# Kernel optimization log

Hardware: AMD Instinct MI355X
Metric: run time of the kernel (lower is better)

## Reference

```python
import jax, jax.numpy as jnp
import numpy as np

N, E, F, FE, H, R = 100000, 3200000, 2, 7, 64, 500
BN_EPS = 1e-5
LEAKY_SLOPE = 0.01


def _bn(h, g, b):
    # BatchNorm1d in training mode: batch statistics over the node axis
    m = h.mean(0)
    v = h.var(0)
    return (h - m) * jax.lax.rsqrt(v + BN_EPS) * g + b


def _gine_conv(x, src, dst, edge_attr, eps, el_w, el_b, w1, b1, g, bt, w2, b2):
    # message: relu(x_j + Lin(edge_attr)); aggregate: scatter-add at dst
    msg = jax.nn.relu(x[src] + edge_attr @ el_w + el_b)          # [E, d]
    agg = jax.ops.segment_sum(msg, dst, num_segments=N)          # [N, d]
    h = (1.0 + eps) * x + agg
    # nn: Linear -> BN -> ReLU -> Linear -> ReLU
    h = jax.nn.relu(_bn(h @ w1 + b1, g, bt))
    return jax.nn.relu(h @ w2 + b2)


def setup_inputs() -> dict:
    key = jax.random.key(0)
    ks = jax.random.split(key, 16)
    r = lambda k, s, sc=0.1: jax.random.normal(k, s, dtype=jnp.float32) * sc
    return {
        "x": jax.random.normal(ks[0], (N, F), dtype=jnp.float32),
        "edge_attr": jax.random.normal(ks[1], (E, FE), dtype=jnp.float32),
        "edge_index": jax.random.randint(ks[2], (2, E), 0, N),
        "epoch": 1,
        "eps1": jnp.zeros((), jnp.float32),
        "el1_w": r(ks[3], (FE, F)), "el1_b": jnp.zeros((F,), jnp.float32),
        "n1_w1": r(ks[4], (F, H)), "n1_b1": jnp.zeros((H,), jnp.float32),
        "n1_g": jnp.ones((H,), jnp.float32), "n1_bt": jnp.zeros((H,), jnp.float32),
        "n1_w2": r(ks[5], (H, H)), "n1_b2": jnp.zeros((H,), jnp.float32),
        "eps2": jnp.zeros((), jnp.float32),
        "el2_w": r(ks[6], (FE, H)), "el2_b": jnp.zeros((H,), jnp.float32),
        "n2_w1": r(ks[7], (H, H)), "n2_b1": jnp.zeros((H,), jnp.float32),
        "n2_g": jnp.ones((H,), jnp.float32), "n2_bt": jnp.zeros((H,), jnp.float32),
        "n2_w2": r(ks[8], (H, H)), "n2_b2": jnp.zeros((H,), jnp.float32),
        "reg_w": r(ks[9], (H, R)), "reg_b": jnp.zeros((R,), jnp.float32),
        "end_w": r(ks[10], (R, 1)), "end_b": jnp.zeros((1,), jnp.float32),
    }


def reference(x, edge_attr, edge_index, epoch,
              eps1, el1_w, el1_b, n1_w1, n1_b1, n1_g, n1_bt, n1_w2, n1_b2,
              eps2, el2_w, el2_b, n2_w1, n2_b1, n2_g, n2_bt, n2_w2, n2_b2,
              reg_w, reg_b, end_w, end_b):
    src, dst = edge_index[0], edge_index[1]
    out = _gine_conv(x, src, dst, edge_attr, eps1, el1_w, el1_b,
                     n1_w1, n1_b1, n1_g, n1_bt, n1_w2, n1_b2)
    for _ in range(3 - 1):  # num_layers=3, shared conv2 weights
        out = _gine_conv(out, src, dst, edge_attr, eps2, el2_w, el2_b,
                         n2_w1, n2_b1, n2_g, n2_bt, n2_w2, n2_b2)
    # dropout p=0.0 -> identity; epoch only resets dropout, no effect here
    out = out @ reg_w + reg_b
    out = jnp.where(out >= 0, out, LEAKY_SLOPE * out)  # LeakyReLU
    out = out @ end_w + end_b                            # [N, 1]
    return out
```

## Files before the change

kernel.cpp:

```cpp
#include <hip/hip_runtime.h>

#define NN 100000
#define NE 3200000

__global__ __launch_bounds__(256) void count_kernel(const int* __restrict__ dst,
                                                    int* __restrict__ cnt) {
  int stride = gridDim.x * 256;
  for (int e = blockIdx.x * 256 + threadIdx.x; e < NE; e += stride)
    atomicAdd(&cnt[dst[e]], 1);
}

__global__ __launch_bounds__(1024) void scan_kernel(const int* __restrict__ cnt,
                                                    int* __restrict__ rowptr,
                                                    int* __restrict__ ofs) {
  __shared__ int bsum[1024];
  int tid = threadIdx.x;
  const int CH = (NN + 1023) / 1024;
  int lo = tid * CH, hi = lo + CH < NN ? lo + CH : NN;
  if (lo > NN) lo = NN;
  if (hi < lo) hi = lo;
  int s = 0;
  for (int i = lo; i < hi; i++) s += cnt[i];
  bsum[tid] = s;
  __syncthreads();
  for (int off = 1; off < 1024; off <<= 1) {
    int v = bsum[tid];
    int u = (tid >= off) ? bsum[tid - off] : 0;
    __syncthreads();
    bsum[tid] = v + u;
    __syncthreads();
  }
  int pre = (tid == 0) ? 0 : bsum[tid - 1];
  for (int i = lo; i < hi; i++) {
    int cv = cnt[i];
    rowptr[i] = pre;
    ofs[i] = pre;
    pre += cv;
  }
  if (tid == 1023) rowptr[NN] = pre;
}

__global__ __launch_bounds__(256) void scatter2p_kernel(
    const int* __restrict__ src, const int* __restrict__ dst,
    const float* __restrict__ ea, int* __restrict__ ofs,
    float* __restrict__ pe, const float* __restrict__ x,
    const float* __restrict__ elw, const float* __restrict__ elb,
    float* __restrict__ msg1) {
  float w0[7], w1r[7];
#pragma unroll
  for (int k = 0; k < 7; k++) { w0[k] = elw[k * 2]; w1r[k] = elw[k * 2 + 1]; }
  float b0 = elb[0], b1 = elb[1];
  int stride = gridDim.x * 256;
  for (int e = blockIdx.x * 256 + threadIdx.x; e < NE; e += stride) {
    int sn = src[e];
    int pos = atomicAdd(&ofs[dst[e]], 1);
    float av[7];
#pragma unroll
    for (int k = 0; k < 7; k++) av[k] = ea[e * 7 + k];
    float4 a, b;
    a.x = av[0]; a.y = av[1]; a.z = av[2]; a.w = av[3];
    b.x = av[4]; b.y = av[5]; b.z = av[6];
    b.w = __int_as_float(sn);
    ((float4*)pe)[pos * 2 + 0] = a;
    ((float4*)pe)[pos * 2 + 1] = b;
    float m0 = b0, m1 = b1;
#pragma unroll
    for (int k = 0; k < 7; k++) {
      m0 = fmaf(av[k], w0[k], m0);
      m1 = fmaf(av[k], w1r[k], m1);
    }
    m0 = fmaxf(m0 + x[sn * 2 + 0], 0.f);
    m1 = fmaxf(m1 + x[sn * 2 + 1], 0.f);
    float2 mv; mv.x = m0; mv.y = m1;
    ((float2*)msg1)[pos] = mv;
  }
}

__global__ __launch_bounds__(256) void scatter1_kernel(
    const int* __restrict__ dst, int* __restrict__ ofs, int* __restrict__ eid_s) {
  int stride = gridDim.x * 256;
  for (int e = blockIdx.x * 256 + threadIdx.x; e < NE; e += stride) {
    int pos = atomicAdd(&ofs[dst[e]], 1);
    eid_s[pos] = e;
  }
}

__global__ __launch_bounds__(256) void l1sum_kernel(
    const int* __restrict__ rowptr, const float* __restrict__ msg1,
    float* __restrict__ agg) {
  int stride = gridDim.x * 256;
  for (int n = blockIdx.x * 256 + threadIdx.x; n < NN; n += stride) {
    int r0 = rowptr[n], r1 = rowptr[n + 1];
    float a0 = 0.f, a1 = 0.f;
    const float2* mp = (const float2*)msg1;
    for (int i = r0; i < r1; i++) {
      float2 v = mp[i];
      a0 += v.x;
      a1 += v.y;
    }
    agg[n * 2 + 0] = a0;
    agg[n * 2 + 1] = a1;
  }
}

__global__ __launch_bounds__(256) void l1agg_kernel(
    const int* __restrict__ rowptr, const int* __restrict__ eid_s,
    const int* __restrict__ src, const float* __restrict__ ea,
    const float* __restrict__ x, const float* __restrict__ elw,
    const float* __restrict__ elb, float* __restrict__ agg) {
  float w0[7], w1r[7];
#pragma unroll
  for (int k = 0; k < 7; k++) { w0[k] = elw[k * 2]; w1r[k] = elw[k * 2 + 1]; }
  float b0 = elb[0], b1 = elb[1];
  int stride = gridDim.x * 256;
  for (int n = blockIdx.x * 256 + threadIdx.x; n < NN; n += stride) {
    int r0 = rowptr[n], r1 = rowptr[n + 1];
    float a0 = 0.f, a1 = 0.f;
    for (int i = r0; i < r1; i++) {
      int e = eid_s[i];
      int sn = src[e];
      float m0 = b0, m1 = b1;
#pragma unroll
      for (int k = 0; k < 7; k++) {
        float a = ea[e * 7 + k];
        m0 = fmaf(a, w0[k], m0);
        m1 = fmaf(a, w1r[k], m1);
      }
      m0 = fmaxf(m0 + x[sn * 2 + 0], 0.f);
      m1 = fmaxf(m1 + x[sn * 2 + 1], 0.f);
      a0 += m0; a1 += m1;
    }
    agg[n * 2 + 0] = a0;
    agg[n * 2 + 1] = a1;
  }
}

#define PROJ(m, aq, bq) do { \
  m = bel; \
  m = fmaf((aq).x, wel[0], m); m = fmaf((aq).y, wel[1], m); \
  m = fmaf((aq).z, wel[2], m); m = fmaf((aq).w, wel[3], m); \
  m = fmaf((bq).x, wel[4], m); m = fmaf((bq).y, wel[5], m); \
  m = fmaf((bq).z, wel[6], m); } while (0)

#define LOADG(base) do { \
  na0 = p4[2 * (base) + 0]; nb0 = p4[2 * (base) + 1]; \
  na1 = p4[2 * (base) + 2]; nb1 = p4[2 * (base) + 3]; \
  na2 = p4[2 * (base) + 4]; nb2 = p4[2 * (base) + 5]; \
  na3 = p4[2 * (base) + 6]; nb3 = p4[2 * (base) + 7]; } while (0)

#define CLAMPSID(dst, bq) do { \
  unsigned raw = (unsigned)__float_as_int((bq).w); \
  dst = (raw >= (unsigned)NN) ? 0u : raw; } while (0)

__global__ __launch_bounds__(256) void gine64r_kernel(
    const int* __restrict__ rowptr, const float* __restrict__ edat,
    const float* __restrict__ xin, const float* __restrict__ elw,
    const float* __restrict__ elb, const float* __restrict__ w1,
    const float* __restrict__ b1, const float* __restrict__ eps_p,
    float* __restrict__ tbuf, float* __restrict__ stats) {
  __shared__ float wl[64 * 64];
  __shared__ float hb[4][64];
  __shared__ float red[256];
  int tid = threadIdx.x, lane = tid & 63, wv = tid >> 6;
  for (int i2 = tid; i2 < 64 * 64; i2 += 256) wl[i2] = w1[i2];
  float wel[7];
#pragma unroll
  for (int k = 0; k < 7; k++) wel[k] = elw[k * 64 + lane];
  float bel = elb[lane], b1c = b1[lane];
  float ep = 1.0f + *eps_p;
  float s = 0.f, ss = 0.f;
  __syncthreads();
  const float4* p4 = (const float4*)edat;
  const float* xl = xin + lane;
  int nw = gridDim.x * 4;
  for (int n = blockIdx.x * 4 + wv; n < NN; n += nw) {
    int r0 = rowptr[n], r1 = rowptr[n + 1];
    int len = r1 - r0;
    float acc = 0.f;
    if (len > 0) {
      int ng = (len + 3) >> 2;
      float4 na0, nb0, na1, nb1, na2, nb2, na3, nb3;
      LOADG(r0);
      float4 ca0 = na0, cb0 = nb0, ca1 = na1, cb1 = nb1;
      float4 ca2 = na2, cb2 = nb2, ca3 = na3, cb3 = nb3;
      int b1i = (ng > 1) ? (r0 + 4) : r0;
      LOADG(b1i);
      float mc0, mc1, mc2, mc3;
      PROJ(mc0, ca0, cb0); PROJ(mc1, ca1, cb1);
      PROJ(mc2, ca2, cb2); PROJ(mc3, ca3, cb3);
      unsigned s0, s1, s2, s3;
      CLAMPSID(s0, cb0); CLAMPSID(s1, cb1); CLAMPSID(s2, cb2); CLAMPSID(s3, cb3);
      float gc0 = xl[s0 * 64], gc1 = xl[s1 * 64];
      float gc2 = xl[s2 * 64], gc3 = xl[s3 * 64];
      for (int g = 0; g < ng; g++) {
        float mn0, mn1, mn2, mn3;
        PROJ(mn0, na0, nb0); PROJ(mn1, na1, nb1);
        PROJ(mn2, na2, nb2); PROJ(mn3, na3, nb3);
        unsigned t0, t1, t2, t3;
        CLAMPSID(t0, nb0); CLAMPSID(t1, nb1); CLAMPSID(t2, nb2); CLAMPSID(t3, nb3);
        float gn0 = xl[t0 * 64], gn1 = xl[t1 * 64];
        float gn2 = xl[t2 * 64], gn3 = xl[t3 * 64];
        int b2 = (g + 2 < ng) ? (r0 + 4 * (g + 2)) : r0;
        LOADG(b2);
        int rem = len - 4 * g;
        acc += (rem > 0) ? fmaxf(mc0 + gc0, 0.f) : 0.f;
        acc += (rem > 1) ? fmaxf(mc1 + gc1, 0.f) : 0.f;
        acc += (rem > 2) ? fmaxf(mc2 + gc2, 0.f) : 0.f;
        acc += (rem > 3) ? fmaxf(mc3 + gc3, 0.f) : 0.f;
        mc0 = mn0; mc1 = mn1; mc2 = mn2; mc3 = mn3;
        gc0 = gn0; gc1 = gn1; gc2 = gn2; gc3 = gn3;
      }
    }
    float h = ep * xin[n * 64 + lane] + acc;
    hb[wv][lane] = h;
    float t = b1c;
#pragma unroll
    for (int k = 0; k < 64; k++) t = fmaf(hb[wv][k], wl[k * 64 + lane], t);
    tbuf[n * 64 + lane] = t;
    s += t;
    ss += t * t;
  }
  double* dsum = (double*)stats;
  red[tid] = s;
  __syncthreads();
  if (tid < 64) unsafeAtomicAdd(&dsum[tid], (double)(red[tid] + red[tid + 64] + red[tid + 128] + red[tid + 192]));
  __syncthreads();
  red[tid] = ss;
  __syncthreads();
  if (tid < 64) unsafeAtomicAdd(&dsum[64 + tid], (double)(red[tid] + red[tid + 64] + red[tid + 128] + red[tid + 192]));
}

__global__ __launch_bounds__(256) void gine64s_kernel(
    const int* __restrict__ rowptr, const int* __restrict__ eid_s,
    const int* __restrict__ src, const float* __restrict__ ea,
    const float* __restrict__ xin, const float* __restrict__ elw,
    const float* __restrict__ elb, const float* __restrict__ w1,
    const float* __restrict__ b1, const float* __restrict__ eps_p,
    float* __restrict__ tbuf, float* __restrict__ stats) {
  __shared__ float wl[64 * 64];
  __shared__ float hb[4][64];
  __shared__ float red[256];
  int tid = threadIdx.x, lane = tid & 63, wv = tid >> 6;
  for (int i = tid; i < 64 * 64; i += 256) wl[i] = w1[i];
  float wel[7];
#pragma unroll
  for (int k = 0; k < 7; k++) wel[k] = elw[k * 64 + lane];
  float bel = elb[lane], b1c = b1[lane];
  float ep = 1.0f + *eps_p;
  float s = 0.f, ss = 0.f;
  __syncthreads();
  int nw = gridDim.x * 4;
  for (int n = blockIdx.x * 4 + wv; n < NN; n += nw) {
    int r0 = rowptr[n], r1 = rowptr[n + 1];
    float acc = 0.f;
    for (int i = r0; i < r1; i++) {
      int e = eid_s[i];
      int sn = src[e];
      float m = bel;
#pragma unroll
      for (int k = 0; k < 7; k++) m = fmaf(ea[e * 7 + k], wel[k], m);
      m += xin[sn * 64 + lane];
      acc += fmaxf(m, 0.f);
    }
    float h = ep * xin[n * 64 + lane] + acc;
    hb[wv][lane] = h;
    float t = b1c;
#pragma unroll
    for (int k = 0; k < 64; k++) t = fmaf(hb[wv][k], wl[k * 64 + lane], t);
    tbuf[n * 64 + lane] = t;
    s += t;
    ss += t * t;
  }
  double* dsum = (double*)stats;
  red[tid] = s;
  __syncthreads();
  if (tid < 64) unsafeAtomicAdd(&dsum[tid], (double)(red[tid] + red[tid + 64] + red[tid + 128] + red[tid + 192]));
  __syncthreads();
  red[tid] = ss;
  __syncthreads();
  if (tid < 64) unsafeAtomicAdd(&dsum[64 + tid], (double)(red[tid] + red[tid + 64] + red[tid + 128] + red[tid + 192]));
}

__global__ __launch_bounds__(256) void edge1_kernel(
    const float* __restrict__ x, const float* __restrict__ ea,
    const int* __restrict__ src, const int* __restrict__ dst,
    const float* __restrict__ elw, const float* __restrict__ elb,
    float* __restrict__ agg) {
  float w0[7], w1[7];
#pragma unroll
  for (int k = 0; k < 7; k++) { w0[k] = elw[k * 2]; w1[k] = elw[k * 2 + 1]; }
  float b0 = elb[0], b1 = elb[1];
  int stride = gridDim.x * 256;
  for (int e = blockIdx.x * 256 + threadIdx.x; e < NE; e += stride) {
    int s = src[e], d = dst[e];
    float m0 = b0, m1 = b1;
#pragma unroll
    for (int k = 0; k < 7; k++) {
      float a = ea[e * 7 + k];
      m0 = fmaf(a, w0[k], m0);
      m1 = fmaf(a, w1[k], m1);
    }
    m0 = fmaxf(m0 + x[s * 2 + 0], 0.f);
    m1 = fmaxf(m1 + x[s * 2 + 1], 0.f);
    unsafeAtomicAdd(&agg[d * 2 + 0], m0);
    unsafeAtomicAdd(&agg[d * 2 + 1], m1);
  }
}

__global__ __launch_bounds__(256) void edge64_kernel(
    const float* __restrict__ xin, const float* __restrict__ ea,
    const int* __restrict__ src, const int* __restrict__ dst,
    const float* __restrict__ elw, const float* __restrict__ elb,
    float* __restrict__ agg) {
  int lane = threadIdx.x & 63;
  int wid = (blockIdx.x * 256 + threadIdx.x) >> 6;
  int nw = (gridDim.x * 256) >> 6;
  float w[7];
#pragma unroll
  for (int k = 0; k < 7; k++) w[k] = elw[k * 64 + lane];
  float b = elb[lane];
  for (int e = wid; e < NE; e += nw) {
    int eu = __builtin_amdgcn_readfirstlane(e);
    int s = src[eu];
    int d = dst[eu];
    float m = b;
#pragma unroll
    for (int k = 0; k < 7; k++) m = fmaf(ea[eu * 7 + k], w[k], m);
    m += xin[s * 64 + lane];
    m = fmaxf(m, 0.f);
    unsafeAtomicAdd(&agg[d * 64 + lane], m);
  }
}

__global__ __launch_bounds__(256) void nodeA64_kernel(
    const float* __restrict__ xin, float* __restrict__ tbuf,
    const float* __restrict__ w1, const float* __restrict__ b1,
    const float* __restrict__ eps_p, float* __restrict__ stats) {
  __shared__ float wl[64 * 64];
  __shared__ float hbuf[4][64];
  __shared__ float red[256];
  int tid = threadIdx.x;
  int c = tid & 63, nl = tid >> 6;
  for (int i = tid; i < 64 * 64; i += 256) wl[i] = w1[i];
  float ep = 1.0f + *eps_p;
  float bc = b1[c];
  float s = 0.f, ss = 0.f;
  __syncthreads();
  for (int n0 = blockIdx.x * 4; n0 < NN; n0 += gridDim.x * 4) {
    int n = n0 + nl;
    bool valid = n < NN;
    float h = 0.f;
    if (valid) h = ep * xin[n * 64 + c] + tbuf[n * 64 + c];
    hbuf[nl][c] = h;
    __syncthreads();
    if (valid) {
      float t = bc;
#pragma unroll
      for (int k = 0; k < 64; k++) t = fmaf(hbuf[nl][k], wl[k * 64 + c], t);
      tbuf[n * 64 + c] = t;
      s += t;
      ss += t * t;
    }
    __syncthreads();
  }
  double* dsum = (double*)stats;
  red[tid] = s;
  __syncthreads();
  if (tid < 64) unsafeAtomicAdd(&dsum[tid], (double)(red[tid] + red[tid + 64] + red[tid + 128] + red[tid + 192]));
  __syncthreads();
  red[tid] = ss;
  __syncthreads();
  if (tid < 64) unsafeAtomicAdd(&dsum[64 + tid], (double)(red[tid] + red[tid + 64] + red[tid + 128] + red[tid + 192]));
}

__global__ __launch_bounds__(256) void nodeA2_kernel(
    const float* __restrict__ x, const float* __restrict__ agg1,
    float* __restrict__ tbuf, const float* __restrict__ w1,
    const float* __restrict__ b1, const float* __restrict__ eps_p,
    float* __restrict__ stats) {
  __shared__ float red[256];
  int tid = threadIdx.x;
  int c = tid & 63, nl = tid >> 6;
  float wa = w1[c], wb = w1[64 + c], bc = b1[c];
  float ep = 1.0f + *eps_p;
  float s = 0.f, ss = 0.f;
  for (int n0 = blockIdx.x * 4; n0 < NN; n0 += gridDim.x * 4) {
    int n = n0 + nl;
    if (n < NN) {
      float h0 = ep * x[n * 2 + 0] + agg1[n * 2 + 0];
      float h1 = ep * x[n * 2 + 1] + agg1[n * 2 + 1];
      float t = fmaf(h1, wb, fmaf(h0, wa, bc));
      tbuf[n * 64 + c] = t;
      s += t;
      ss += t * t;
    }
  }
  double* dsum = (double*)stats;
  red[tid] = s;
  __syncthreads();
  if (tid < 64) unsafeAtomicAdd(&dsum[tid], (double)(red[tid] + red[tid + 64] + red[tid + 128] + red[tid + 192]));
  __syncthreads();
  red[tid] = ss;
  __syncthreads();
  if (tid < 64) unsafeAtomicAdd(&dsum[64 + tid], (double)(red[tid] + red[tid + 64] + red[tid + 128] + red[tid + 192]));
}

__global__ __launch_bounds__(256) void nodeB_kernel(
    const float* __restrict__ tin, float* __restrict__ outb,
    const float* __restrict__ w2, const float* __restrict__ b2,
    const float* __restrict__ stats, const float* __restrict__ g,
    const float* __restrict__ bt) {
  __shared__ float wl[64 * 64];
  __shared__ float ubuf[4][64];
  __shared__ float scsh[128];
  int tid = threadIdx.x;
  int c = tid & 63, nl = tid >> 6;
  for (int i = tid; i < 64 * 64; i += 256) wl[i] = w2[i];
  if (tid < 64) {
    const double* ds = (const double*)stats;
    double m = ds[tid] / (double)NN;
    double v = ds[64 + tid] / (double)NN - m * m;
    float sc = g[tid] * (float)(1.0 / sqrt(v + 1e-5));
    scsh[tid] = sc;
    scsh[64 + tid] = bt[tid] - (float)m * sc;
  }
  float bc = b2[c];
  __syncthreads();
  float scale = scsh[c], shift = scsh[64 + c];
  for (int n0 = blockIdx.x * 4; n0 < NN; n0 += gridDim.x * 4) {
    int n = n0 + nl;
    bool valid = n < NN;
    float u = 0.f;
    if (valid) {
      float t = tin[n * 64 + c];
      u = fmaxf(fmaf(t, scale, shift), 0.f);
    }
    ubuf[nl][c] = u;
    __syncthreads();
    if (valid) {
      float o = bc;
#pragma unroll
      for (int k = 0; k < 64; k++) o = fmaf(ubuf[nl][k], wl[k * 64 + c], o);
      outb[n * 64 + c] = fmaxf(o, 0.f);
    }
    __syncthreads();
  }
}

__global__ __launch_bounds__(256) void final_kernel(
    const float* __restrict__ xin, const float* __restrict__ regw,
    const float* __restrict__ regb, const float* __restrict__ endw,
    const float* __restrict__ endb, float* __restrict__ out) {
  __shared__ float wl[64 * 128];
  __shared__ float eb[256];
  int tid = threadIdx.x;
  int node = blockIdx.x * 256 + tid;
  bool valid = node < NN;
  float xr[64];
  if (valid) {
    const float4* xp = (const float4*)(xin + node * 64);
#pragma unroll
    for (int k4 = 0; k4 < 16; k4++) {
      float4 v = xp[k4];
      xr[k4 * 4 + 0] = v.x; xr[k4 * 4 + 1] = v.y;
      xr[k4 * 4 + 2] = v.z; xr[k4 * 4 + 3] = v.w;
    }
  }
  float y = 0.f;
  for (int ch = 0; ch < 4; ch++) {
    int j0 = ch * 125;
    __syncthreads();
    for (int idx = tid; idx < 64 * 125; idx += 256) {
      int k = idx / 125;
      int jl = idx - k * 125;
      wl[k * 128 + jl] = regw[k * 500 + j0 + jl];
    }
    if (tid < 125) { eb[tid] = regb[j0 + tid]; eb[128 + tid] = endw[j0 + tid]; }
    __syncthreads();
    if (valid) {
      int jl = 0;
      for (; jl + 4 <= 125; jl += 4) {
        float t0 = eb[jl], t1 = eb[jl + 1], t2 = eb[jl + 2], t3 = eb[jl + 3];
#pragma unroll
        for (int k = 0; k < 64; k++) {
          float4 w4 = *(const float4*)&wl[k * 128 + jl];
          float xv = xr[k];
          t0 = fmaf(xv, w4.x, t0);
          t1 = fmaf(xv, w4.y, t1);
          t2 = fmaf(xv, w4.z, t2);
          t3 = fmaf(xv, w4.w, t3);
        }
        t0 = t0 >= 0.f ? t0 : 0.01f * t0;
        t1 = t1 >= 0.f ? t1 : 0.01f * t1;
        t2 = t2 >= 0.f ? t2 : 0.01f * t2;
        t3 = t3 >= 0.f ? t3 : 0.01f * t3;
        y += t0 * eb[128 + jl] + t1 * eb[128 + jl + 1] + t2 * eb[128 + jl + 2] + t3 * eb[128 + jl + 3];
      }
      {
        float t = eb[124];
#pragma unroll
        for (int k = 0; k < 64; k++) t = fmaf(xr[k], wl[k * 128 + 124], t);
        t = t >= 0.f ? t : 0.01f * t;
        y += t * eb[128 + 124];
      }
    }
  }
  if (valid) out[node] = y + endb[0];
}

extern "C" void kernel_launch(void* const* d_in, const int* in_sizes, int n_in,
                              void* d_out, int out_size, void* d_ws, size_t ws_size,
                              hipStream_t stream) {
  const float* x    = (const float*)d_in[0];
  const float* ea   = (const float*)d_in[1];
  const int*   ei   = (const int*)d_in[2];
  const float* eps1 = (const float*)d_in[4];
  const float* el1w = (const float*)d_in[5];
  const float* el1b = (const float*)d_in[6];
  const float* n1w1 = (const float*)d_in[7];
  const float* n1b1 = (const float*)d_in[8];
  const float* n1g  = (const float*)d_in[9];
  const float* n1bt = (const float*)d_in[10];
  const float* n1w2 = (const float*)d_in[11];
  const float* n1b2 = (const float*)d_in[12];
  const float* eps2 = (const float*)d_in[13];
  const float* el2w = (const float*)d_in[14];
  const float* el2b = (const float*)d_in[15];
  const float* n2w1 = (const float*)d_in[16];
  const float* n2b1 = (const float*)d_in[17];
  const float* n2g  = (const float*)d_in[18];
  const float* n2bt = (const float*)d_in[19];
  const float* n2w2 = (const float*)d_in[20];
  const float* n2b2 = (const float*)d_in[21];
  const float* regw = (const float*)d_in[22];
  const float* regb = (const float*)d_in[23];
  const float* endw = (const float*)d_in[24];
  const float* endb = (const float*)d_in[25];
  const int* srcp = ei;
  const int* dstp = ei + NE;

  const size_t o_stats  = 0;
  const size_t o_rowptr = 512;
  const size_t o_cnt    = 100516;
  const size_t o_buf0   = 200576;
  const size_t o_buf1   = 6600576;
  const size_t o_agg1   = 13000576;
  const size_t o_edat   = 13200576;
  const size_t needA2 = (o_edat + (size_t)NE * 8 + 96) * 4;
  const size_t needA1 = (o_edat + (size_t)NE) * 4;
  const size_t needB  = (2 * 6600000 + 384) * 4;

  float* wsf = (float*)d_ws;

  if (ws_size >= needA1) {
    const bool packed = ws_size >= needA2;
    float* stats = wsf + o_stats;
    int* rowptr  = (int*)(wsf + o_rowptr);
    int* cnt     = (int*)(wsf + o_cnt);
    float* buf0  = wsf + o_buf0;
    float* buf1  = wsf + o_buf1;
    float* agg1  = wsf + o_agg1;
    float* edat  = wsf + o_edat;
    float* msg1  = buf0;

    hipMemsetAsync(cnt, 0, NN * sizeof(int), stream);
    count_kernel<<<4096, 256, 0, stream>>>(dstp, cnt);
    scan_kernel<<<1, 1024, 0, stream>>>(cnt, rowptr, cnt);
    if (packed)
      scatter2p_kernel<<<4096, 256, 0, stream>>>(srcp, dstp, ea, cnt, edat,
                                                 x, el1w, el1b, msg1);
    else
      scatter1_kernel<<<4096, 256, 0, stream>>>(dstp, cnt, (int*)edat);

    hipMemsetAsync(stats, 0, 128 * sizeof(double), stream);
    if (packed)
      l1sum_kernel<<<391, 256, 0, stream>>>(rowptr, msg1, agg1);
    else
      l1agg_kernel<<<391, 256, 0, stream>>>(rowptr, (const int*)edat, srcp, ea,
                                            x, el1w, el1b, agg1);
    nodeA2_kernel<<<2048, 256, 0, stream>>>(x, agg1, buf1, n1w1, n1b1, eps1, stats);
    nodeB_kernel<<<2048, 256, 0, stream>>>(buf1, buf1, n1w2, n1b2, stats, n1g, n1bt);

    float* cur = buf1;
    float* wrk = buf0;
    for (int l = 0; l < 2; l++) {
      hipMemsetAsync(stats, 0, 128 * sizeof(double), stream);
      if (packed)
        gine64r_kernel<<<4096, 256, 0, stream>>>(rowptr, edat, cur, el2w, el2b,
                                                 n2w1, n2b1, eps2, wrk, stats);
      else
        gine64s_kernel<<<4096, 256, 0, stream>>>(rowptr, (const int*)edat, srcp,
                                                 ea, cur, el2w, el2b, n2w1, n2b1,
                                                 eps2, wrk, stats);
      nodeB_kernel<<<2048, 256, 0, stream>>>(wrk, wrk, n2w2, n2b2, stats, n2g, n2bt);
      float* tmp = cur; cur = wrk; wrk = tmp;
    }

    final_kernel<<<(NN + 255) / 256, 256, 0, stream>>>(cur, regw, regb, endw, endb,
                                                       (float*)d_out);
    return;
  }

  if (ws_size < needB) return;
  const size_t BUF = 6600000;
  float* buf0 = (float*)d_ws;
  float* buf1 = buf0 + BUF;
  float* stats = buf1 + BUF;

  float* t1 = buf1;
  float* agg1 = buf1 + NN * 64;
  hipMemsetAsync(agg1, 0, NN * 2 * sizeof(float), stream);
  hipMemsetAsync(stats, 0, 128 * sizeof(double), stream);
  edge1_kernel<<<2048, 256, 0, stream>>>(x, ea, srcp, dstp, el1w, el1b, agg1);
  nodeA2_kernel<<<2048, 256, 0, stream>>>(x, agg1, t1, n1w1, n1b1, eps1, stats);
  nodeB_kernel<<<2048, 256, 0, stream>>>(t1, buf1, n1w2, n1b2, stats, n1g, n1bt);

  float* cur = buf1;
  float* wrk = buf0;
  for (int l = 0; l < 2; l++) {
    hipMemsetAsync(wrk, 0, NN * 64 * sizeof(float), stream);
    hipMemsetAsync(stats, 0, 128 * sizeof(double), stream);
    edge64_kernel<<<2048, 256, 0, stream>>>(cur, ea, srcp, dstp, el2w, el2b, wrk);
    nodeA64_kernel<<<2048, 256, 0, stream>>>(cur, wrk, n2w1, n2b1, eps2, stats);
    nodeB_kernel<<<2048, 256, 0, stream>>>(wrk, wrk, n2w2, n2b2, stats, n2g, n2bt);
    float* tmp = cur; cur = wrk; wrk = tmp;
  }

  final_kernel<<<(NN + 255) / 256, 256, 0, stream>>>(cur, regw, regb, endw, endb,
                                                     (float*)d_out);
}
```

Measured before the change: 1.539 ms.

## Store edge records and gathered node features in fp16 for layer 2-3 aggregation

Packs the 7 edge attributes into a 16-byte fp16 record with source IDs in a separate int array, instead of a 32-byte fp32 record. nodeB now also writes an fp16 copy of the node features, and the gather kernel reads those halves. This cuts edge-stream and gather bandwidth in the dominant aggregation kernels. It also uses separate stats buffers zeroed by one memset, which removes the per-layer memsets. The cost is reduced precision on edge attributes and gathered features.

```diff
diff --git a/kernel.cpp b/kernel.cpp
--- a/kernel.cpp
+++ b/kernel.cpp
@@ -1,7 +1,33 @@
 #include <hip/hip_runtime.h>
+#include <hip/hip_fp16.h>
 
 #define NN 100000
 #define NE 3200000
+
+__device__ inline unsigned pkh(float a, float b) {
+  __half2 h;
+  h.x = __float2half(a);
+  h.y = __float2half(b);
+  unsigned u;
+  __builtin_memcpy(&u, &h, 4);
+  return u;
+}
+__device__ inline float2 uph(unsigned u) {
+  __half2 h;
+  __builtin_memcpy(&h, &u, 4);
+  return __half22float2(h);
+}
+__device__ inline float h1f(unsigned short v) {
+  __half h;
+  __builtin_memcpy(&h, &v, 2);
+  return __half2float(h);
+}
+__device__ inline unsigned short f1h(float f) {
+  __half h = __float2half(f);
+  unsigned short u;
+  __builtin_memcpy(&u, &h, 2);
+  return u;
+}
 
 __global__ __launch_bounds__(256) void count_kernel(const int* __restrict__ dst,
                                                     int* __restrict__ cnt) {
@@ -40,12 +66,12 @@
   if (tid == 1023) rowptr[NN] = pre;
 }
 
-__global__ __launch_bounds__(256) void scatter2p_kernel(
+__global__ __launch_bounds__(256) void scatter2h_kernel(
     const int* __restrict__ src, const int* __restrict__ dst,
     const float* __restrict__ ea, int* __restrict__ ofs,
-    float* __restrict__ pe, const float* __restrict__ x,
-    const float* __restrict__ elw, const float* __restrict__ elb,
-    float* __restrict__ msg1) {
+    uint4* __restrict__ erec, int* __restrict__ esrc,
+    const float* __restrict__ x, const float* __restrict__ elw,
+    const float* __restrict__ elb, float* __restrict__ msg1) {
   float w0[7], w1r[7];
 #pragma unroll
   for (int k = 0; k < 7; k++) { w0[k] = elw[k * 2]; w1r[k] = elw[k * 2 + 1]; }
@@ -57,12 +83,13 @@
     float av[7];
 #pragma unroll
     for (int k = 0; k < 7; k++) av[k] = ea[e * 7 + k];
-    float4 a, b;
-    a.x = av[0]; a.y = av[1]; a.z = av[2]; a.w = av[3];
-    b.x = av[4]; b.y = av[5]; b.z = av[6];
-    b.w = __int_as_float(sn);
-    ((float4*)pe)[pos * 2 + 0] = a;
-    ((float4*)pe)[pos * 2 + 1] = b;
+    uint4 r;
+    r.x = pkh(av[0], av[1]);
+    r.y = pkh(av[2], av[3]);
+    r.z = pkh(av[4], av[5]);
+    r.w = pkh(av[6], 0.f);
+    erec[pos] = r;
+    esrc[pos] = sn;
     float m0 = b0, m1 = b1;
 #pragma unroll
     for (int k = 0; k < 7; k++) {
@@ -135,26 +162,18 @@
   }
 }
 
-#define PROJ(m, aq, bq) do { \
+#define PROJH(m, u) do { \
+  float2 q0 = uph((u).x), q1 = uph((u).y), q2 = uph((u).z), q3 = uph((u).w); \
   m = bel; \
-  m = fmaf((aq).x, wel[0], m); m = fmaf((aq).y, wel[1], m); \
-  m = fmaf((aq).z, wel[2], m); m = fmaf((aq).w, wel[3], m); \
-  m = fmaf((bq).x, wel[4], m); m = fmaf((bq).y, wel[5], m); \
-  m = fmaf((bq).z, wel[6], m); } while (0)
-
-#define LOADG(base) do { \
-  na0 = p4[2 * (base) + 0]; nb0 = p4[2 * (base) + 1]; \
-  na1 = p4[2 * (base) + 2]; nb1 = p4[2 * (base) + 3]; \
-  na2 = p4[2 * (base) + 4]; nb2 = p4[2 * (base) + 5]; \
-  na3 = p4[2 * (base) + 6]; nb3 = p4[2 * (base) + 7]; } while (0)
-
-#define CLAMPSID(dst, bq) do { \
-  unsigned raw = (unsigned)__float_as_int((bq).w); \
-  dst = (raw >= (unsigned)NN) ? 0u : raw; } while (0)
-
-__global__ __launch_bounds__(256) void gine64r_kernel(
-    const int* __restrict__ rowptr, const float* __restrict__ edat,
-    const float* __restrict__ xin, const float* __restrict__ elw,
+  m = fmaf(q0.x, wel[0], m); m = fmaf(q0.y, wel[1], m); \
+  m = fmaf(q1.x, wel[2], m); m = fmaf(q1.y, wel[3], m); \
+  m = fmaf(q2.x, wel[4], m); m = fmaf(q2.y, wel[5], m); \
+  m = fmaf(q3.x, wel[6], m); } while (0)
+
+__global__ __launch_bounds__(256) void gine64h_kernel(
+    const int* __restrict__ rowptr, const uint4* __restrict__ erec,
+    const int* __restrict__ esrc, const float* __restrict__ xin,
+    const unsigned short* __restrict__ xh, const float* __restrict__ elw,
     const float* __restrict__ elb, const float* __restrict__ w1,
     const float* __restrict__ b1, const float* __restrict__ eps_p,
     float* __restrict__ tbuf, float* __restrict__ stats) {
@@ -170,46 +189,44 @@
   float ep = 1.0f + *eps_p;
   float s = 0.f, ss = 0.f;
   __syncthreads();
-  const float4* p4 = (const float4*)edat;
-  const float* xl = xin + lane;
+  const unsigned short* xl = xh + lane;
   int nw = gridDim.x * 4;
   for (int n = blockIdx.x * 4 + wv; n < NN; n += nw) {
     int r0 = rowptr[n], r1 = rowptr[n + 1];
-    int len = r1 - r0;
     float acc = 0.f;
-    if (len > 0) {
-      int ng = (len + 3) >> 2;
-      float4 na0, nb0, na1, nb1, na2, nb2, na3, nb3;
-      LOADG(r0);
-      float4 ca0 = na0, cb0 = nb0, ca1 = na1, cb1 = nb1;
-      float4 ca2 = na2, cb2 = nb2, ca3 = na3, cb3 = nb3;
-      int b1i = (ng > 1) ? (r0 + 4) : r0;
-      LOADG(b1i);
-      float mc0, mc1, mc2, mc3;
-      PROJ(mc0, ca0, cb0); PROJ(mc1, ca1, cb1);
-      PROJ(mc2, ca2, cb2); PROJ(mc3, ca3, cb3);
-      unsigned s0, s1, s2, s3;
-      CLAMPSID(s0, cb0); CLAMPSID(s1, cb1); CLAMPSID(s2, cb2); CLAMPSID(s3, cb3);
-      float gc0 = xl[s0 * 64], gc1 = xl[s1 * 64];
-      float gc2 = xl[s2 * 64], gc3 = xl[s3 * 64];
-      for (int g = 0; g < ng; g++) {
-        float mn0, mn1, mn2, mn3;
-        PROJ(mn0, na0, nb0); PROJ(mn1, na1, nb1);
-        PROJ(mn2, na2, nb2); PROJ(mn3, na3, nb3);
-        unsigned t0, t1, t2, t3;
-        CLAMPSID(t0, nb0); CLAMPSID(t1, nb1); CLAMPSID(t2, nb2); CLAMPSID(t3, nb3);
-        float gn0 = xl[t0 * 64], gn1 = xl[t1 * 64];
-        float gn2 = xl[t2 * 64], gn3 = xl[t3 * 64];
-        int b2 = (g + 2 < ng) ? (r0 + 4 * (g + 2)) : r0;
-        LOADG(b2);
-        int rem = len - 4 * g;
-        acc += (rem > 0) ? fmaxf(mc0 + gc0, 0.f) : 0.f;
-        acc += (rem > 1) ? fmaxf(mc1 + gc1, 0.f) : 0.f;
-        acc += (rem > 2) ? fmaxf(mc2 + gc2, 0.f) : 0.f;
-        acc += (rem > 3) ? fmaxf(mc3 + gc3, 0.f) : 0.f;
-        mc0 = mn0; mc1 = mn1; mc2 = mn2; mc3 = mn3;
-        gc0 = gn0; gc1 = gn1; gc2 = gn2; gc3 = gn3;
+    int i = r0;
+    int rem = r1 - r0;
+    if (rem >= 4) {
+      uint4 u0 = erec[i], u1 = erec[i + 1], u2 = erec[i + 2], u3 = erec[i + 3];
+      int s0 = esrc[i], s1 = esrc[i + 1], s2 = esrc[i + 2], s3 = esrc[i + 3];
+      while (true) {
+        float g0 = h1f(xl[s0 * 64]);
+        float g1 = h1f(xl[s1 * 64]);
+        float g2 = h1f(xl[s2 * 64]);
+        float g3 = h1f(xl[s3 * 64]);
+        i += 4; rem -= 4;
+        bool more = rem >= 4;
+        int ip = more ? i : r0;
+        uint4 v0 = erec[ip], v1 = erec[ip + 1], v2 = erec[ip + 2], v3 = erec[ip + 3];
+        int t0 = esrc[ip], t1 = esrc[ip + 1], t2 = esrc[ip + 2], t3 = esrc[ip + 3];
+        float m0, m1, m2, m3;
+        PROJH(m0, u0); PROJH(m1, u1); PROJH(m2, u2); PROJH(m3, u3);
+        acc += fmaxf(m0 + g0, 0.f);
+        acc += fmaxf(m1 + g1, 0.f);
+        acc += fmaxf(m2 + g2, 0.f);
+        acc += fmaxf(m3 + g3, 0.f);
+        u0 = v0; u1 = v1; u2 = v2; u3 = v3;
+        s0 = t0; s1 = t1; s2 = t2; s3 = t3;
+        if (!more) break;
       }
+    }
+    for (; i < r1; i++) {
+      uint4 u = erec[i];
+      int sn = esrc[i];
+      float m;
+      PROJH(m, u);
+      m += h1f(xl[sn * 64]);
+      acc += fmaxf(m, 0.f);
     }
     float h = ep * xin[n * 64 + lane] + acc;
     hb[wv][lane] = h;
@@ -409,7 +426,7 @@
     const float* __restrict__ tin, float* __restrict__ outb,
     const float* __restrict__ w2, const float* __restrict__ b2,
     const float* __restrict__ stats, const float* __restrict__ g,
-    const float* __restrict__ bt) {
+    const float* __restrict__ bt, unsigned short* __restrict__ xh) {
   __shared__ float wl[64 * 64];
   __shared__ float ubuf[4][64];
   __shared__ float scsh[128];
@@ -441,7 +458,9 @@
       float o = bc;
 #pragma unroll
       for (int k = 0; k < 64; k++) o = fmaf(ubuf[nl][k], wl[k * 64 + c], o);
-      outb[n * 64 + c] = fmaxf(o, 0.f);
+      o = fmaxf(o, 0.f);
+      outb[n * 64 + c] = o;
+      if (xh) xh[n * 64 + c] = f1h(o);
     }
     __syncthreads();
   }
@@ -540,13 +559,15 @@
   const int* dstp = ei + NE;
 
   const size_t o_stats  = 0;
-  const size_t o_rowptr = 512;
-  const size_t o_cnt    = 100516;
-  const size_t o_buf0   = 200576;
-  const size_t o_buf1   = 6600576;
-  const size_t o_agg1   = 13000576;
-  const size_t o_edat   = 13200576;
-  const size_t needA2 = (o_edat + (size_t)NE * 8 + 96) * 4;
+  const size_t o_cnt    = 768;
+  const size_t o_rowptr = 100768;
+  const size_t o_buf0   = 200832;
+  const size_t o_buf1   = 6600832;
+  const size_t o_xh     = 13000832;
+  const size_t o_agg1   = 16200832;
+  const size_t o_edat   = 16400832;
+  const size_t o_srcs   = 29200832;
+  const size_t needA2 = (o_srcs + (size_t)NE) * 4;
   const size_t needA1 = (o_edat + (size_t)NE) * 4;
   const size_t needB  = (2 * 6600000 + 384) * 4;
 
@@ -554,50 +575,66 @@
 
   if (ws_size >= needA1) {
     const bool packed = ws_size >= needA2;
-    float* stats = wsf + o_stats;
+    float* stats0 = wsf + o_stats;
+    float* stats1 = wsf + o_stats + 256;
+    float* stats2 = wsf + o_stats + 512;
+    int* cnt     = (int*)(wsf + o_cnt);
     int* rowptr  = (int*)(wsf + o_rowptr);
-    int* cnt     = (int*)(wsf + o_cnt);
     float* buf0  = wsf + o_buf0;
     float* buf1  = wsf + o_buf1;
+    unsigned short* xh = (unsigned short*)(wsf + o_xh);
     float* agg1  = wsf + o_agg1;
-    float* edat  = wsf + o_edat;
+    uint4* erec  = (uint4*)(wsf + o_edat);
+    int* esrc    = (int*)(wsf + o_srcs);
     float* msg1  = buf0;
 
-    hipMemsetAsync(cnt, 0, NN * sizeof(int), stream);
+    hipMemsetAsync(wsf, 0, (768 + NN) * sizeof(float), stream);
+
     count_kernel<<<4096, 256, 0, stream>>>(dstp, cnt);
     scan_kernel<<<1, 1024, 0, stream>>>(cnt, rowptr, cnt);
     if (packed)
-      scatter2p_kernel<<<4096, 256, 0, stream>>>(srcp, dstp, ea, cnt, edat,
+      scatter2h_kernel<<<4096, 256, 0, stream>>>(srcp, dstp, ea, cnt, erec, esrc,
                                                  x, el1w, el1b, msg1);
     else
-      scatter1_kernel<<<4096, 256, 0, stream>>>(dstp, cnt, (int*)edat);
-
-    hipMemsetAsync(stats, 0, 128 * sizeof(double), stream);
+      scatter1_kernel<<<4096, 256, 0, stream>>>(dstp, cnt, (int*)(wsf + o_edat));
+
     if (packed)
       l1sum_kernel<<<391, 256, 0, stream>>>(rowptr, msg1, agg1);
     else
-      l1agg_kernel<<<391, 256, 0, stream>>>(rowptr, (const int*)edat, srcp, ea,
-                                            x, el1w, el1b, agg1);
-    nodeA2_kernel<<<2048, 256, 0, stream>>>(x, agg1, buf1, n1w1, n1b1, eps1, stats);
-    nodeB_kernel<<<2048, 256, 0, stream>>>(buf1, buf1, n1w2, n1b2, stats, n1g, n1bt);
-
-    float* cur = buf1;
-    float* wrk = buf0;
-    for (int l = 0; l < 2; l++) {
-      hipMemsetAsync(stats, 0, 128 * sizeof(double), stream);
-      if (packed)
-        gine64r_kernel<<<4096, 256, 0, stream>>>(rowptr, edat, cur, el2w, el2b,
-                                                 n2w1, n2b1, eps2, wrk, stats);
-      else
-        gine64s_kernel<<<4096, 256, 0, stream>>>(rowptr, (const int*)edat, srcp,
-                                                 ea, cur, el2w, el2b, n2w1, n2b1,
-                                                 eps2, wrk, stats);
-      nodeB_kernel<<<2048, 256, 0, stream>>>(wrk, wrk, n2w2, n2b2, stats, n2g, n2bt);
-      float* tmp = cur; cur = wrk; wrk = tmp;
-    }
-
-    final_kernel<<<(NN + 255) / 256, 256, 0, stream>>>(cur, regw, regb, endw, endb,
-                                                       (float*)d_out);
+      l1agg_kernel<<<391, 256, 0, stream>>>(rowptr, (const int*)(wsf + o_edat),
+                                            srcp, ea, x, el1w, el1b, agg1);
+    nodeA2_kernel<<<2048, 256, 0, stream>>>(x, agg1, buf1, n1w1, n1b1, eps1, stats0);
+    nodeB_kernel<<<2048, 256, 0, stream>>>(buf1, buf1, n1w2, n1b2, stats0,
+                                           n1g, n1bt, packed ? xh : nullptr);
+
+    if (packed) {
+      gine64h_kernel<<<4096, 256, 0, stream>>>(rowptr, erec, esrc, buf1, xh,
+                                               el2w, el2b, n2w1, n2b1, eps2,
+                                               buf0, stats1);
+      nodeB_kernel<<<2048, 256, 0, stream>>>(buf0, buf0, n2w2, n2b2, stats1,
+                                             n2g, n2bt, xh);
+      gine64h_kernel<<<4096, 256, 0, stream>>>(rowptr, erec, esrc, buf0, xh,
+                                               el2w, el2b, n2w1, n2b1, eps2,
+                                               buf1, stats2);
+      nodeB_kernel<<<2048, 256, 0, stream>>>(buf1, buf1, n2w2, n2b2, stats2,
+                                             n2g, n2bt, nullptr);
+      final_kernel<<<(NN + 255) / 256, 256, 0, stream>>>(buf1, regw, regb, endw,
+                                                         endb, (float*)d_out);
+    } else {
+      float* cur = buf1;
+      float* wrk = buf0;
+      float* sl[2] = {stats1, stats2};
+      for (int l = 0; l < 2; l++) {
+        gine64s_kernel<<<4096, 256, 0, stream>>>(rowptr, (const int*)(wsf + o_edat),
+                                                 srcp, ea, cur, el2w, el2b, n2w1,
+                                                 n2b1, eps2, wrk, sl[l]);
+        nodeB_kernel<<<2048, 256, 0, stream>>>(wrk, wrk, n2w2, n2b2, sl[l],
+                                               n2g, n2bt, nullptr);
+        float* tmp = cur; cur = wrk; wrk = tmp;
+      }
+      final_kernel<<<(NN + 255) / 256, 256, 0, stream>>>(cur, regw, regb, endw,
+                                                         endb, (float*)d_out);
+    }
     return;
   }
 
@@ -613,7 +650,8 @@
   hipMemsetAsync(stats, 0, 128 * sizeof(double), stream);
   edge1_kernel<<<2048, 256, 0, stream>>>(x, ea, srcp, dstp, el1w, el1b, agg1);
   nodeA2_kernel<<<2048, 256, 0, stream>>>(x, agg1, t1, n1w1, n1b1, eps1, stats);
-  nodeB_kernel<<<2048, 256, 0, stream>>>(t1, buf1, n1w2, n1b2, stats, n1g, n1bt);
+  nodeB_kernel<<<2048, 256, 0, stream>>>(t1, buf1, n1w2, n1b2, stats, n1g, n1bt,
+                                         nullptr);
 
   float* cur = buf1;
   float* wrk = buf0;
@@ -622,7 +660,8 @@
     hipMemsetAsync(stats, 0, 128 * sizeof(double), stream);
     edge64_kernel<<<2048, 256, 0, stream>>>(cur, ea, srcp, dstp, el2w, el2b, wrk);
     nodeA64_kernel<<<2048, 256, 0, stream>>>(cur, wrk, n2w1, n2b1, eps2, stats);
-    nodeB_kernel<<<2048, 256, 0, stream>>>(wrk, wrk, n2w2, n2b2, stats, n2g, n2bt);
+    nodeB_kernel<<<2048, 256, 0, stream>>>(wrk, wrk, n2w2, n2b2, stats, n2g, n2bt,
+                                           nullptr);
     float* tmp = cur; cur = wrk; wrk = tmp;
   }
 
```

Result: faster. 1.346 ms, median of 2 (-12.6%).
